# Kernel optimization log

Hardware: AMD Instinct MI355X
Metric: run time of the kernel (lower is better)

## Reference

```python
import jax, jax.numpy as jnp
import numpy as np

N, L = 8192, 4096
AFWD = 0.999
EPS = 1e-05


def setup_inputs() -> dict:
    key = jax.random.key(0)
    x = jax.random.normal(key, (N, L), dtype=jnp.float32)
    mu0 = jnp.zeros((L,), dtype=jnp.float32)   # buffer m, init 0
    var0 = jnp.ones((L,), dtype=jnp.float32)   # buffer var, init 1
    return {"x": x, "mu0": mu0, "var0": var0}


def reference(x, mu0, var0):
    """Online Normalization forward (training mode): sequential per-sample
    EMA mean/variance recurrence over the batch dim.
      y_t   = (x_t - mu_{t-1}) / sqrt(var_{t-1} + eps)
      var_t = afwd*var_{t-1} + afwd*(1-afwd)*(x_t - mu_{t-1})^2
      mu_t  = afwd*mu_{t-1} + (1-afwd)*x_t
    """
    def step(carry, xt):
        mu, var = carry                      # [L], [L]
        scale = jnp.sqrt(var + EPS)          # [L]
        d = xt - mu                          # [L]
        out = d / scale
        var = AFWD * var + AFWD * (1.0 - AFWD) * d * d
        mu = mu + (1.0 - AFWD) * d           # == afwd*mu + (1-afwd)*x
        return (mu, var), out

    (_, _), out = jax.lax.scan(step, (mu0, var0), x)  # out: [N, L]
    return out
```

## Files before the change

### kernel.cpp

```cpp
#include <hip/hip_runtime.h>
#include <math.h>

static constexpr float AFWD = 0.999f;
static constexpr float EPS  = 1e-5f;

typedef float vfloat4 __attribute__((ext_vector_type(4)));

__global__ __launch_bounds__(256) void onlnorm_pass1(
    const float* __restrict__ x, float* __restrict__ Sv,
    float* __restrict__ T0v, float* __restrict__ Ev, int n, int L)
{
    const int chunk = blockIdx.y;
    const int col = (blockIdx.x * blockDim.x + threadIdx.x) * 4;
    if (col >= L) return;
    const float a = AFWD, b = 1.0f - AFWD, ab = AFWD * (1.0f - AFWD);
    const float* xp = x + (size_t)chunk * (size_t)n * L + col;

    float m0=0.f,m1=0.f,m2=0.f,m3=0.f;
    float t0=0.f,t1=0.f,t2=0.f,t3=0.f;
    float e0=0.f,e1=0.f,e2=0.f,e3=0.f;

    constexpr int PF = 8;

#define P1_STEP(xv)                                                   \
    do { float d;                                                     \
        d = (xv).x - m0; e0 += d; t0 = a*t0 + ab*d*d; m0 += b*d;      \
        d = (xv).y - m1; e1 += d; t1 = a*t1 + ab*d*d; m1 += b*d;      \
        d = (xv).z - m2; e2 += d; t2 = a*t2 + ab*d*d; m2 += b*d;      \
        d = (xv).w - m3; e3 += d; t3 = a*t3 + ab*d*d; m3 += b*d;      \
    } while (0)

    if ((n % PF) == 0 && n >= 2 * PF) {
        float4 buf[PF];
        #pragma unroll
        for (int j = 0; j < PF; ++j)
            buf[j] = *reinterpret_cast<const float4*>(xp + (size_t)j * L);
        for (int i0 = 0; i0 + PF < n; i0 += PF) {
            #pragma unroll
            for (int j = 0; j < PF; ++j) {
                const float4 xv = buf[j];
                buf[j] = *reinterpret_cast<const float4*>(xp + (size_t)(i0 + PF + j) * L);
                P1_STEP(xv);
            }
        }
        #pragma unroll
        for (int j = 0; j < PF; ++j) { const float4 xv = buf[j]; P1_STEP(xv); }
    } else {
        for (int i = 0; i < n; ++i) {
            const float4 xv = *reinterpret_cast<const float4*>(xp + (size_t)i * L);
            P1_STEP(xv);
        }
    }
#undef P1_STEP

    const size_t base = (size_t)chunk * L + col;
    *reinterpret_cast<float4*>(Sv  + base) = make_float4(m0,m1,m2,m3);
    *reinterpret_cast<float4*>(T0v + base) = make_float4(t0,t1,t2,t3);
    *reinterpret_cast<float4*>(Ev  + base) = make_float4(e0,e1,e2,e3);
}

__global__ __launch_bounds__(64) void onlnorm_pass2(
    const float* __restrict__ Sv, const float* __restrict__ T0v,
    const float* __restrict__ Ev, const float* __restrict__ mu0,
    const float* __restrict__ var0, float* __restrict__ muin,
    float* __restrict__ varin, int C, int L, float A, float B, float W)
{
    const int col = blockIdx.x * blockDim.x + threadIdx.x;
    if (col >= L) return;
    float mu = mu0[col], var = var0[col];
    constexpr int BATCH = 8;
    float sb[BATCH], tb[BATCH], eb[BATCH];
    int c0 = 0;
    for (; c0 + BATCH <= C; c0 += BATCH) {
        #pragma unroll
        for (int j = 0; j < BATCH; ++j) {
            const size_t idx = (size_t)(c0 + j) * L + col;
            sb[j] = Sv[idx]; tb[j] = T0v[idx]; eb[j] = Ev[idx];
        }
        #pragma unroll
        for (int j = 0; j < BATCH; ++j) {
            const size_t idx = (size_t)(c0 + j) * L + col;
            muin[idx]  = mu;
            varin[idx] = var;
            var = A*var + tb[j] - 2.0f*B*mu*eb[j] + W*mu*mu;
            mu  = A*mu + sb[j];
        }
    }
    for (; c0 < C; ++c0) {
        const size_t idx = (size_t)c0 * L + col;
        muin[idx] = mu; varin[idx] = var;
        const float s = Sv[idx], t = T0v[idx], e = Ev[idx];
        var = A*var + t - 2.0f*B*mu*e + W*mu*mu;
        mu  = A*mu + s;
    }
}

__global__ __launch_bounds__(256) void onlnorm_pass3(
    const float* __restrict__ x, const float* __restrict__ muin,
    const float* __restrict__ varin, float* __restrict__ out, int n, int L)
{
    const int chunk = blockIdx.y;
    const int col = (blockIdx.x * blockDim.x + threadIdx.x) * 4;
    if (col >= L) return;
    const float a = AFWD, b = 1.0f - AFWD, ab = AFWD * (1.0f - AFWD);
    const size_t cbase = (size_t)chunk * L + col;
    const float4 muv  = *reinterpret_cast<const float4*>(muin  + cbase);
    const float4 varv = *reinterpret_cast<const float4*>(varin + cbase);
    float m0=muv.x, m1=muv.y, m2=muv.z, m3=muv.w;
    float v0=varv.x, v1=varv.y, v2=varv.z, v3=varv.w;
    const float* xp = x   + (size_t)chunk * (size_t)n * L + col;
    float*       op = out + (size_t)chunk * (size_t)n * L + col;

    constexpr int PF = 8;

#define P3_STEP(xv, row)                                                        \
    do { vfloat4 ov; float d;                                                   \
        d = (xv).x - m0; ov.x = d * rsqrtf(v0 + EPS); v0 = a*v0 + ab*d*d; m0 += b*d; \
        d = (xv).y - m1; ov.y = d * rsqrtf(v1 + EPS); v1 = a*v1 + ab*d*d; m1 += b*d; \
        d = (xv).z - m2; ov.z = d * rsqrtf(v2 + EPS); v2 = a*v2 + ab*d*d; m2 += b*d; \
        d = (xv).w - m3; ov.w = d * rsqrtf(v3 + EPS); v3 = a*v3 + ab*d*d; m3 += b*d; \
        __builtin_nontemporal_store(ov, reinterpret_cast<vfloat4*>(op + (size_t)(row) * L)); \
    } while (0)

    if ((n % PF) == 0 && n >= 2 * PF) {
        float4 buf[PF];
        #pragma unroll
        for (int j = 0; j < PF; ++j)
            buf[j] = *reinterpret_cast<const float4*>(xp + (size_t)j * L);
        for (int i0 = 0; i0 + PF < n; i0 += PF) {
            #pragma unroll
            for (int j = 0; j < PF; ++j) {
                const float4 xv = buf[j];
                buf[j] = *reinterpret_cast<const float4*>(xp + (size_t)(i0 + PF + j) * L);
                P3_STEP(xv, i0 + j);
            }
        }
        const int ie = n - PF;
        #pragma unroll
        for (int j = 0; j < PF; ++j) { const float4 xv = buf[j]; P3_STEP(xv, ie + j); }
    } else {
        for (int i = 0; i < n; ++i) {
            const float4 xv = *reinterpret_cast<const float4*>(xp + (size_t)i * L);
            P3_STEP(xv, i);
        }
    }
#undef P3_STEP
}

extern "C" void kernel_launch(void* const* d_in, const int* in_sizes, int n_in,
                              void* d_out, int out_size, void* d_ws, size_t ws_size,
                              hipStream_t stream) {
    const float* x    = (const float*)d_in[0];
    const float* mu0  = (const float*)d_in[1];
    const float* var0 = (const float*)d_in[2];
    float* out = (float*)d_out;

    const int L = in_sizes[1];
    const int N = in_sizes[0] / L;

    int C = 256;
    while (C > 1 && ((size_t)5 * (size_t)C * L * sizeof(float) > ws_size ||
                     (N % C) != 0 || ((N / C) % 8) != 0))
        C >>= 1;
    const int n = N / C;

    float* Sv    = (float*)d_ws;
    float* T0v   = Sv    + (size_t)C * L;
    float* Ev    = T0v   + (size_t)C * L;
    float* muin  = Ev    + (size_t)C * L;
    float* varin = muin  + (size_t)C * L;

    const double a  = (double)AFWD;
    const double An = pow(a, (double)n);
    const float A = (float)An;
    const float B = (float)(An * (1.0 - a));
    const float W = (float)(An * (1.0 - An));

    const dim3 blk(256);
    const dim3 g1((L / 4 + 255) / 256, C);

    onlnorm_pass1<<<g1, blk, 0, stream>>>(x, Sv, T0v, Ev, n, L);
    onlnorm_pass2<<<dim3((L + 63) / 64), dim3(64), 0, stream>>>(
        Sv, T0v, Ev, mu0, var0, muin, varin, C, L, A, B, W);
    onlnorm_pass3<<<g1, blk, 0, stream>>>(x, muin, varin, out, n, L);
}
```

Measured before the change: 86.64 us.

## Fuse chunk-prefix scan into output pass, dropping the separate scan kernel

The standalone cross-chunk scan kernel is removed. Each output block now redundantly recomputes the prefix combination of chunk summaries up to its own chunk before running its chunk's recurrence, which eliminates one launch and the muin/varin round trip through memory. The chunk count drops from 256 to 64 so that the redundant prefix work per block stays small, at the cost of longer serial chunks and fewer blocks in the parallel passes.

```diff
diff --git a/kernel.cpp b/kernel.cpp
--- a/kernel.cpp
+++ b/kernel.cpp
@@ -6,7 +6,7 @@
 
 typedef float vfloat4 __attribute__((ext_vector_type(4)));
 
-__global__ __launch_bounds__(256) void onlnorm_pass1(
+__global__ __launch_bounds__(256) void onlnorm_passA(
     const float* __restrict__ x, float* __restrict__ Sv,
     float* __restrict__ T0v, float* __restrict__ Ev, int n, int L)
 {
@@ -59,55 +59,51 @@
     *reinterpret_cast<float4*>(Ev  + base) = make_float4(e0,e1,e2,e3);
 }
 
-__global__ __launch_bounds__(64) void onlnorm_pass2(
+__global__ __launch_bounds__(256) void onlnorm_passB(
+    const float* __restrict__ x,
     const float* __restrict__ Sv, const float* __restrict__ T0v,
-    const float* __restrict__ Ev, const float* __restrict__ mu0,
-    const float* __restrict__ var0, float* __restrict__ muin,
-    float* __restrict__ varin, int C, int L, float A, float B, float W)
-{
-    const int col = blockIdx.x * blockDim.x + threadIdx.x;
-    if (col >= L) return;
-    float mu = mu0[col], var = var0[col];
-    constexpr int BATCH = 8;
-    float sb[BATCH], tb[BATCH], eb[BATCH];
-    int c0 = 0;
-    for (; c0 + BATCH <= C; c0 += BATCH) {
-        #pragma unroll
-        for (int j = 0; j < BATCH; ++j) {
-            const size_t idx = (size_t)(c0 + j) * L + col;
-            sb[j] = Sv[idx]; tb[j] = T0v[idx]; eb[j] = Ev[idx];
-        }
-        #pragma unroll
-        for (int j = 0; j < BATCH; ++j) {
-            const size_t idx = (size_t)(c0 + j) * L + col;
-            muin[idx]  = mu;
-            varin[idx] = var;
-            var = A*var + tb[j] - 2.0f*B*mu*eb[j] + W*mu*mu;
-            mu  = A*mu + sb[j];
-        }
-    }
-    for (; c0 < C; ++c0) {
-        const size_t idx = (size_t)c0 * L + col;
-        muin[idx] = mu; varin[idx] = var;
-        const float s = Sv[idx], t = T0v[idx], e = Ev[idx];
-        var = A*var + t - 2.0f*B*mu*e + W*mu*mu;
-        mu  = A*mu + s;
-    }
-}
-
-__global__ __launch_bounds__(256) void onlnorm_pass3(
-    const float* __restrict__ x, const float* __restrict__ muin,
-    const float* __restrict__ varin, float* __restrict__ out, int n, int L)
+    const float* __restrict__ Ev,
+    const float* __restrict__ mu0, const float* __restrict__ var0,
+    float* __restrict__ out,
+    int n, int L, float A, float B, float W)
 {
     const int chunk = blockIdx.y;
     const int col = (blockIdx.x * blockDim.x + threadIdx.x) * 4;
     if (col >= L) return;
+
+    vfloat4 mu4  = *reinterpret_cast<const vfloat4*>(mu0  + col);
+    vfloat4 var4 = *reinterpret_cast<const vfloat4*>(var0 + col);
+    {
+        constexpr int BATCH = 4;
+        vfloat4 sb[BATCH], tb[BATCH], eb[BATCH];
+        int c0 = 0;
+        for (; c0 + BATCH <= chunk; c0 += BATCH) {
+            #pragma unroll
+            for (int j = 0; j < BATCH; ++j) {
+                const size_t idx = (size_t)(c0 + j) * L + col;
+                sb[j] = *reinterpret_cast<const vfloat4*>(Sv  + idx);
+                tb[j] = *reinterpret_cast<const vfloat4*>(T0v + idx);
+                eb[j] = *reinterpret_cast<const vfloat4*>(Ev  + idx);
+            }
+            #pragma unroll
+            for (int j = 0; j < BATCH; ++j) {
+                var4 = A*var4 + tb[j] - 2.0f*B*mu4*eb[j] + W*mu4*mu4;
+                mu4  = A*mu4 + sb[j];
+            }
+        }
+        for (; c0 < chunk; ++c0) {
+            const size_t idx = (size_t)c0 * L + col;
+            const vfloat4 s = *reinterpret_cast<const vfloat4*>(Sv  + idx);
+            const vfloat4 t = *reinterpret_cast<const vfloat4*>(T0v + idx);
+            const vfloat4 e = *reinterpret_cast<const vfloat4*>(Ev  + idx);
+            var4 = A*var4 + t - 2.0f*B*mu4*e + W*mu4*mu4;
+            mu4  = A*mu4 + s;
+        }
+    }
+    float m0=mu4.x, m1=mu4.y, m2=mu4.z, m3=mu4.w;
+    float v0=var4.x, v1=var4.y, v2=var4.z, v3=var4.w;
+
     const float a = AFWD, b = 1.0f - AFWD, ab = AFWD * (1.0f - AFWD);
-    const size_t cbase = (size_t)chunk * L + col;
-    const float4 muv  = *reinterpret_cast<const float4*>(muin  + cbase);
-    const float4 varv = *reinterpret_cast<const float4*>(varin + cbase);
-    float m0=muv.x, m1=muv.y, m2=muv.z, m3=muv.w;
-    float v0=varv.x, v1=varv.y, v2=varv.z, v3=varv.w;
     const float* xp = x   + (size_t)chunk * (size_t)n * L + col;
     float*       op = out + (size_t)chunk * (size_t)n * L + col;
 
@@ -158,17 +154,15 @@
     const int L = in_sizes[1];
     const int N = in_sizes[0] / L;
 
-    int C = 256;
-    while (C > 1 && ((size_t)5 * (size_t)C * L * sizeof(float) > ws_size ||
-                     (N % C) != 0 || ((N / C) % 8) != 0))
+    int C = 64;
+    while (C > 1 && ((size_t)3 * (size_t)C * L * sizeof(float) > ws_size ||
+                     (N % C) != 0 || ((N / C) % 16) != 0))
         C >>= 1;
     const int n = N / C;
 
     float* Sv    = (float*)d_ws;
     float* T0v   = Sv    + (size_t)C * L;
     float* Ev    = T0v   + (size_t)C * L;
-    float* muin  = Ev    + (size_t)C * L;
-    float* varin = muin  + (size_t)C * L;
 
     const double a  = (double)AFWD;
     const double An = pow(a, (double)n);
@@ -179,8 +173,7 @@
     const dim3 blk(256);
     const dim3 g1((L / 4 + 255) / 256, C);
 
-    onlnorm_pass1<<<g1, blk, 0, stream>>>(x, Sv, T0v, Ev, n, L);
-    onlnorm_pass2<<<dim3((L + 63) / 64), dim3(64), 0, stream>>>(
-        Sv, T0v, Ev, mu0, var0, muin, varin, C, L, A, B, W);
-    onlnorm_pass3<<<g1, blk, 0, stream>>>(x, muin, varin, out, n, L);
+    onlnorm_passA<<<g1, blk, 0, stream>>>(x, Sv, T0v, Ev, n, L);
+    onlnorm_passB<<<g1, blk, 0, stream>>>(x, Sv, T0v, Ev, mu0, var0, out,
+                                          n, L, A, B, W);
 }
```

Measured after the change: 95.98 us. 10.8% more time.
